# Kernel optimization log

Hardware: AMD Instinct MI355X
Metric: run time of the kernel (lower is better)

## Reference

```python
import jax, jax.numpy as jnp
import numpy as np

N, Lq, Lk = 4, 4096, 4096
H, P = 16, 128
D = H * P  # 2048


def setup_inputs() -> dict:
    key = jax.random.key(0)
    ks = jax.random.split(key, 7)
    s = 1.0 / np.sqrt(D).astype(np.float32)
    query = jax.random.normal(ks[0], (N, Lq, D), jnp.float32)
    key_t = jax.random.normal(ks[1], (N, Lk, D), jnp.float32)
    Wq = jax.random.normal(ks[2], (D, D), jnp.float32) * s
    Wk = jax.random.normal(ks[3], (D, D), jnp.float32) * s
    Wv = jax.random.normal(ks[4], (D, D), jnp.float32) * s
    query_padding_mask = jax.random.uniform(ks[5], (N, Lq)) < 0.1
    key_padding_mask = jax.random.uniform(ks[6], (N, Lk)) < 0.1
    return {"query": query, "key": key_t, "Wq": Wq, "Wk": Wk, "Wv": Wv,
            "query_padding_mask": query_padding_mask,
            "key_padding_mask": key_padding_mask}


def reference(query, key, Wq, Wk, Wv, query_padding_mask, key_padding_mask):
    n, lq, _ = query.shape
    lk = key.shape[1]
    # torch.nn.Linear(bias=False): y = x @ W^T; split into heads -> (N,H,L,P)
    q = (query @ Wq.T).reshape(n, lq, H, P).transpose(0, 2, 1, 3)
    k = (key @ Wk.T).reshape(n, lk, H, P).transpose(0, 2, 1, 3)
    v = (key @ Wv.T).reshape(n, lk, H, P).transpose(0, 2, 1, 3)
    # _log_exp_kernel(x) = log(1 + exp(x)) = softplus
    pq = jax.nn.softplus(q)
    pk = jax.nn.softplus(k)
    # zero out padded keys so they contribute nothing to numerator/denominator
    pk = jnp.where(key_padding_mask[:, None, :, None], 0.0, pk)
    # linear attention: O(L*d^2) instead of O(L^2*d)
    kv = jnp.einsum("nhkd,nhke->nhde", pk, v)          # (N,H,P,P)
    num = jnp.einsum("nhqd,nhde->nhqe", pq, kv)        # (N,H,Lq,P)
    den = jnp.einsum("nhqd,nhd->nhq", pq, pk.sum(axis=2))[..., None]
    att = num / den
    out = att.transpose(0, 2, 1, 3).reshape(n, lq, H * P)
    # zero out padded query positions
    out = jnp.where(query_padding_mask[..., None], 0.0, out)
    return out
```

## Files before the change

kernel.cpp:

```cpp
#include <hip/hip_runtime.h>
#include <stdint.h>

typedef __attribute__((ext_vector_type(8))) short    bh8;
typedef __attribute__((ext_vector_type(4))) float    fx4;
typedef __attribute__((ext_vector_type(4))) float    f4v;
typedef unsigned short u16;
typedef __attribute__((ext_vector_type(4))) unsigned short u16x4;

#define DEV static __device__ __forceinline__

DEV u16 f2bf(float f) {
  unsigned u = __float_as_uint(f);
  u += 0x7FFFu + ((u >> 16) & 1u);
  return (u16)(u >> 16);
}
DEV float bf2f(u16 s) { return __uint_as_float(((unsigned)s) << 16); }
DEV float softplus_f(float x) { return fmaxf(x, 0.f) + log1pf(expf(-fabsf(x))); }

DEV void gload_lds16(const u16* g, u16* l) {
  __builtin_amdgcn_global_load_lds(
      (const __attribute__((address_space(1))) unsigned int*)g,
      (__attribute__((address_space(3))) unsigned int*)l, 16, 0, 0);
}
DEV void stage2(const u16* s, u16* d) {
  gload_lds16(s, d);
  gload_lds16(s + 131072, d + 4096);
}

__global__ __launch_bounds__(256) void k_cvt(const float* __restrict__ in,
                                             u16* __restrict__ out, int n4) {
  int i = blockIdx.x * 256 + threadIdx.x;
  int stride = gridDim.x * 256;
  for (; i < n4; i += stride) {
    f4v v = ((const f4v*)in)[i];
    u16x4 o;
    o.x = f2bf(v.x); o.y = f2bf(v.y); o.z = f2bf(v.z); o.w = f2bf(v.w);
    ((u16x4*)out)[i] = o;
  }
}


#define MM(a, b, c) __builtin_amdgcn_mfma_f32_16x16x32_bf16(a, b, c, 0, 0, 0)
#define LD(BASE, RR, KS) \
  (*(const bh8*)&lsg[(BASE) + (RR) * 64 + ((((KS) * 32) + ko8) ^ swz)])

#define DECLQ(Q)                                                          \
  fx4 acc##Q##00 = {}, acc##Q##01 = {}, acc##Q##10 = {}, acc##Q##11 = {}, \
      acc##Q##20 = {}, acc##Q##21 = {}, acc##Q##30 = {}, acc##Q##31 = {}

#define WN
#define WV6 asm volatile("s_waitcnt vmcnt(6)");
#define WV4 asm volatile("s_waitcnt vmcnt(4)");

#define LDA4(AB, KS)                                                     \
  a_0##KS = LD(AB, arow0,      KS); a_1##KS = LD(AB, arow0 + 16, KS);    \
  a_2##KS = LD(AB, arow0 + 32, KS); a_3##KS = LD(AB, arow0 + 48, KS);

#define LDB2(BN, BB, KS)                                                 \
  b##BN##_0##KS = LD(BB, brow0,      KS);                                \
  b##BN##_1##KS = LD(BB, brow0 + 16, KS);

#define MFMA8(Q, BN, KS)                                                 \
  acc##Q##00 = MM(a_0##KS, b##BN##_0##KS, acc##Q##00);                   \
  acc##Q##01 = MM(a_0##KS, b##BN##_1##KS, acc##Q##01);                   \
  acc##Q##10 = MM(a_1##KS, b##BN##_0##KS, acc##Q##10);                   \
  acc##Q##11 = MM(a_1##KS, b##BN##_1##KS, acc##Q##11);                   \
  acc##Q##20 = MM(a_2##KS, b##BN##_0##KS, acc##Q##20);                   \
  acc##Q##21 = MM(a_2##KS, b##BN##_1##KS, acc##Q##21);                   \
  acc##Q##30 = MM(a_3##KS, b##BN##_0##KS, acc##Q##30);                   \
  acc##Q##31 = MM(a_3##KS, b##BN##_1##KS, acc##Q##31);

#define PH(MFMAS, WAITS, ...) {                 \
  __VA_ARGS__                                   \
  __builtin_amdgcn_s_barrier();                 \
  __builtin_amdgcn_s_setprio(1);                \
  MFMAS                                         \
  __builtin_amdgcn_s_setprio(0);                \
  WAITS                                         \
  __builtin_amdgcn_s_barrier();                 \
}

#define STE(AC, EL, JOFF) {                                                   \
  float v = AC.EL;                                                            \
  if (EPI >= 1) v = softplus_f(v);                                            \
  if (EPI == 2) { if (mask[gi0 + JOFF]) v = 0.f; }                            \
  C[(size_t)(gi0 + JOFF) * 2048 + gj] = f2bf(v);                              \
}
#define ST1(AC, QR, QC, MI, NI) {                                             \
  int gi0 = bm0 + (QR) * 128 + wr * 64 + (MI) * 16 + (lane >> 4) * 4;         \
  int gj  = bn0 + (QC) * 128 + wc * 32 + (NI) * 16 + l15;                     \
  STE(AC, x, 0) STE(AC, y, 1) STE(AC, z, 2) STE(AC, w, 3)                     \
}
#define EPIQ(Q, QR, QC)                                                       \
  ST1(acc##Q##00, QR, QC, 0, 0) ST1(acc##Q##01, QR, QC, 0, 1)                 \
  ST1(acc##Q##10, QR, QC, 1, 0) ST1(acc##Q##11, QR, QC, 1, 1)                 \
  ST1(acc##Q##20, QR, QC, 2, 0) ST1(acc##Q##21, QR, QC, 2, 1)                 \
  ST1(acc##Q##30, QR, QC, 3, 0) ST1(acc##Q##31, QR, QC, 3, 1)

template <int EPI>
__global__ __launch_bounds__(512, 2) void k_gemm256(
    const u16* __restrict__ A, const u16* __restrict__ B, u16* __restrict__ C,
    const int* __restrict__ mask) {
  extern __shared__ u16 lsg[];
  int tid = threadIdx.x, lane = tid & 63, wid = tid >> 6;
  int xcd = blockIdx.x & 7, i = blockIdx.x >> 3;
  int bm0 = (xcd * 8 + (i & 7)) << 8;
  int bn0 = (i >> 3) << 8;
  int wr = wid >> 2, wc = wid & 3;
  int l15 = lane & 15, ko8 = (lane >> 4) * 8;
  int swz = (l15 & 7) << 3;
  int arow0 = wr * 64 + l15, brow0 = wc * 32 + l15;
  int lr = lane >> 3, cg = (lane & 7) ^ lr;
  const u16* srcA = A + (size_t)(bm0 + wid * 8 + lr) * 2048 + cg * 8;
  const u16* srcB = B + (size_t)(bn0 + wid * 8 + lr) * 2048 + cg * 8;
  u16* lsu = lsg + wid * 512;

  DECLQ(0); DECLQ(1); DECLQ(2); DECLQ(3);
  bh8 a_00 = {}, a_01 = {}, a_10 = {}, a_11 = {},
      a_20 = {}, a_21 = {}, a_30 = {}, a_31 = {};
  bh8 b0_00 = {}, b0_01 = {}, b0_10 = {}, b0_11 = {};
  bh8 b1_00 = {}, b1_01 = {}, b1_10 = {}, b1_11 = {};

  stage2(srcA, lsu + 0);
  stage2(srcB, lsu + 16384);
  stage2(srcB + 262144, lsu + 24576);
  stage2(srcA + 262144, lsu + 8192);
  stage2(srcA + 64, lsu + 32768);
  stage2(srcB + 64, lsu + 49152);
  stage2(srcB + 262144 + 64, lsu + 57344);
  asm volatile("s_waitcnt vmcnt(8)");
  __builtin_amdgcn_s_barrier();
  LDA4(0, 0) LDB2(0, 16384, 0) LDB2(1, 24576, 0)

  for (int it = 0; it < 16; it++) {
    int t1 = 2 * it + 1;
    int t2 = (2 * it + 2) & 31;
    int t3 = (2 * it + 3) & 31;
    PH(MFMA8(0, 0, 0) MFMA8(1, 1, 0), WV6,
       LDA4(0, 1) LDB2(0, 16384, 1) LDB2(1, 24576, 1))
    PH(MFMA8(0, 0, 1) MFMA8(1, 1, 1), WN,
       LDA4(8192, 0) stage2(srcA + 262144 + t1 * 64, lsu + 40960);)
    PH(MFMA8(2, 0, 0) MFMA8(3, 1, 0), WV4,
       LDA4(8192, 1) stage2(srcA + t2 * 64, lsu + 0);)
    PH(MFMA8(2, 0, 1) MFMA8(3, 1, 1), WN,
       LDA4(32768, 0) LDB2(0, 49152, 0) LDB2(1, 57344, 0)
       stage2(srcB + t2 * 64, lsu + 16384);)
    PH(MFMA8(0, 0, 0) MFMA8(1, 1, 0), WV6,
       LDA4(32768, 1) LDB2(0, 49152, 1) LDB2(1, 57344, 1)
       stage2(srcB + 262144 + t2 * 64, lsu + 24576);)
    PH(MFMA8(0, 0, 1) MFMA8(1, 1, 1), WN,
       LDA4(40960, 0) stage2(srcA + 262144 + t2 * 64, lsu + 8192);)
    PH(MFMA8(2, 0, 0) MFMA8(3, 1, 0), WV6,
       LDA4(40960, 1) stage2(srcA + t3 * 64, lsu + 32768);
       stage2(srcB + t3 * 64, lsu + 49152);)
    PH(MFMA8(2, 0, 1) MFMA8(3, 1, 1), WN,
       LDA4(0, 0) LDB2(0, 16384, 0) LDB2(1, 24576, 0)
       stage2(srcB + 262144 + t3 * 64, lsu + 57344);)
  }

  EPIQ(0, 0, 0)
  EPIQ(1, 0, 1)
  EPIQ(2, 1, 0)
  EPIQ(3, 1, 1)
}

__global__ __launch_bounds__(256, 2) void k_kv2(const u16* __restrict__ pk,
                                                const u16* __restrict__ v,
                                                float* __restrict__ part,
                                                float* __restrict__ spart) {
  int nh = blockIdx.x >> 3, slab = blockIdx.x & 7;
  int n = nh >> 4, h = nh & 15;
  __shared__ u16 lsA[128 * 32];
  __shared__ u16 lsB[128 * 32];
  __shared__ float redS[32][128];
  int tid = threadIdx.x, lane = tid & 63, wid = tid >> 6;
  int wr = wid >> 1, wc = wid & 1;
  int kk = tid >> 3;
  int dg = (tid & 7) * 16;
  size_t rowbase = ((size_t)(n * 4096 + slab * 512) + kk) * 2048 + h * 128 + dg;
  int r = lane & 15, ko = (lane >> 4) * 8;
  fx4 acc[4][4] = {};
  float sA[16];
#pragma unroll
  for (int i = 0; i < 16; i++) sA[i] = 0.f;
  for (int k0 = 0; k0 < 512; k0 += 32) {
    __syncthreads();
    bh8 a0 = *(const bh8*)(pk + rowbase + (size_t)k0 * 2048);
    bh8 a1 = *(const bh8*)(pk + rowbase + (size_t)k0 * 2048 + 8);
    bh8 b0 = *(const bh8*)(v + rowbase + (size_t)k0 * 2048);
    bh8 b1 = *(const bh8*)(v + rowbase + (size_t)k0 * 2048 + 8);
#pragma unroll
    for (int i = 0; i < 8; i++) {
      sA[i] += bf2f((u16)a0[i]);
      sA[8 + i] += bf2f((u16)a1[i]);
    }
#pragma unroll
    for (int i = 0; i < 8; i++) {
      lsA[(dg + i) * 32 + kk] = (u16)a0[i];
      lsA[(dg + 8 + i) * 32 + kk] = (u16)a1[i];
      lsB[(dg + i) * 32 + kk] = (u16)b0[i];
      lsB[(dg + 8 + i) * 32 + kk] = (u16)b1[i];
    }
    __syncthreads();
    bh8 af[4], bfr[4];
#pragma unroll
    for (int mi = 0; mi < 4; mi++)
      af[mi] = *(const bh8*)&lsA[(wr * 64 + mi * 16 + r) * 32 + ko];
#pragma unroll
    for (int ni = 0; ni < 4; ni++)
      bfr[ni] = *(const bh8*)&lsB[(wc * 64 + ni * 16 + r) * 32 + ko];
#pragma unroll
    for (int mi = 0; mi < 4; mi++)
#pragma unroll
      for (int ni = 0; ni < 4; ni++)
        acc[mi][ni] = __builtin_amdgcn_mfma_f32_16x16x32_bf16(af[mi], bfr[ni],
                                                              acc[mi][ni], 0, 0, 0);
  }
#pragma unroll
  for (int mi = 0; mi < 4; mi++)
#pragma unroll
    for (int ni = 0; ni < 4; ni++)
#pragma unroll
      for (int j = 0; j < 4; j++) {
        int d = wr * 64 + mi * 16 + (lane >> 4) * 4 + j;
        int e = wc * 64 + ni * 16 + (lane & 15);
        part[(size_t)blockIdx.x * 16384 + e * 128 + d] = acc[mi][ni][j];
      }
#pragma unroll
  for (int i = 0; i < 16; i++) redS[kk][dg + i] = sA[i];
  __syncthreads();
  if (tid < 128) {
    float s = 0.f;
#pragma unroll
    for (int p = 0; p < 32; p++) s += redS[p][tid];
    spart[blockIdx.x * 128 + tid] = s;
  }
}

__global__ __launch_bounds__(256) void k_red(const float* __restrict__ part,
                                             const float* __restrict__ spart,
                                             u16* __restrict__ kvT,
                                             float* __restrict__ sb) {
  int nh = blockIdx.x, tid = threadIdx.x;
  for (int i = tid; i < 16384; i += 256) {
    float s = 0.f;
#pragma unroll
    for (int sl = 0; sl < 8; sl++) s += part[(size_t)(nh * 8 + sl) * 16384 + i];
    kvT[(size_t)nh * 16384 + i] = f2bf(s);
  }
  if (tid < 128) {
    float s = 0.f;
#pragma unroll
    for (int sl = 0; sl < 8; sl++) s += spart[(nh * 8 + sl) * 128 + tid];
    sb[nh * 128 + tid] = s;
  }
}

__global__ __launch_bounds__(256, 2) void k_att(
    const u16* __restrict__ pq, const u16* __restrict__ kvT,
    const float* __restrict__ s, const int* __restrict__ qmask,
    float* __restrict__ out) {
  int b = blockIdx.x;
  int lt = b & 31, h = (b >> 5) & 15, nb = b >> 9;
  int l0 = lt * 128;
  __shared__ u16 lsQ[128 * 128];
  __shared__ u16 lsKV[128 * 128];
  __shared__ float lsS[128];
  __shared__ float lsDen[128];
  int tid = threadIdx.x, lane = tid & 63, wid = tid >> 6;

  int row = tid >> 1, part = tid & 1;
  const u16* gq = pq + ((size_t)(nb * 4096 + l0 + row)) * 2048 + h * 128 + part * 64;
  const u16* gk = kvT + ((size_t)(nb * 16 + h) * 128 + row) * 128 + part * 64;
  int sw = (row & 7) << 3;
#pragma unroll
  for (int j = 0; j < 8; j++) {
    bh8 vq = *(const bh8*)(gq + j * 8);
    bh8 vk = *(const bh8*)(gk + j * 8);
    int ci = (part * 64 + j * 8) ^ sw;
    *(bh8*)&lsQ[row * 128 + ci] = vq;
    *(bh8*)&lsKV[row * 128 + ci] = vk;
  }
  if (tid < 128) lsS[tid] = s[(nb * 16 + h) * 128 + tid];
  __syncthreads();

  if (tid < 128) {
    int rr = tid, swr = (rr & 7) << 3;
    float dsum = 0.f;
    for (int dd = 0; dd < 128; dd++) {
      int d = (dd + rr) & 127;
      dsum += bf2f(lsQ[rr * 128 + (d ^ swr)]) * lsS[d];
    }
    lsDen[rr] = dsum;
  }
  __syncthreads();

  int wr = wid >> 1, wc = wid & 1;
  int r = lane & 15, ko = (lane >> 4) * 8;
  fx4 acc[4][4] = {};
#pragma unroll
  for (int ks = 0; ks < 4; ks++) {
    bh8 af[4], bfr[4];
#pragma unroll
    for (int mi = 0; mi < 4; mi++) {
      int rw = wr * 64 + mi * 16 + r;
      af[mi] = *(const bh8*)&lsQ[rw * 128 + ((ks * 32 + ko) ^ ((rw & 7) << 3))];
    }
#pragma unroll
    for (int ni = 0; ni < 4; ni++) {
      int rw = wc * 64 + ni * 16 + r;
      bfr[ni] = *(const bh8*)&lsKV[rw * 128 + ((ks * 32 + ko) ^ ((rw & 7) << 3))];
    }
#pragma unroll
    for (int mi = 0; mi < 4; mi++)
#pragma unroll
      for (int ni = 0; ni < 4; ni++)
        acc[mi][ni] = __builtin_amdgcn_mfma_f32_16x16x32_bf16(af[mi], bfr[ni],
                                                              acc[mi][ni], 0, 0, 0);
  }
#pragma unroll
  for (int mi = 0; mi < 4; mi++)
#pragma unroll
    for (int ni = 0; ni < 4; ni++)
#pragma unroll
      for (int j = 0; j < 4; j++) {
        int li = wr * 64 + mi * 16 + (lane >> 4) * 4 + j;
        int e = wc * 64 + ni * 16 + (lane & 15);
        int l = l0 + li;
        float v = qmask[nb * 4096 + l] ? 0.f : acc[mi][ni][j] / lsDen[li];
        out[((size_t)(nb * 4096 + l)) * 2048 + h * 128 + e] = v;
      }
}

extern "C" void kernel_launch(void* const* d_in, const int* in_sizes, int n_in,
                              void* d_out, int out_size, void* d_ws, size_t ws_size,
                              hipStream_t stream) {
  const float* query = (const float*)d_in[0];
  const float* key   = (const float*)d_in[1];
  const float* Wq    = (const float*)d_in[2];
  const float* Wk    = (const float*)d_in[3];
  const float* Wv    = (const float*)d_in[4];
  const int* qmask   = (const int*)d_in[5];
  const int* kmask   = (const int*)d_in[6];
  float* out = (float*)d_out;
  char* ws = (char*)d_ws;

  u16* qb   = (u16*)(ws + 0);
  u16* kb   = (u16*)(ws + 67108864ull);
  u16* Wqb  = (u16*)(ws + 134217728ull);
  u16* Wkb  = (u16*)(ws + 142606336ull);
  u16* Wvb  = (u16*)(ws + 150994944ull);
  u16* pq   = (u16*)(ws + 159383552ull);
  u16* kvT  = (u16*)(ws + 226492416ull);
  float* sb = (float*)(ws + 228589568ull);
  float* kvpart = (float*)(ws + 0);
  float* spart  = (float*)(ws + 33554432ull);
  u16* pk = (u16*)d_out;
  u16* vb = (u16*)d_out + 33554432ull;

  k_cvt<<<2048, 256, 0, stream>>>(query, qb, 33554432 / 4);
  k_cvt<<<2048, 256, 0, stream>>>(key, kb, 33554432 / 4);
  k_cvt<<<512, 256, 0, stream>>>(Wq, Wqb, 4194304 / 4);
  k_cvt<<<512, 256, 0, stream>>>(Wk, Wkb, 4194304 / 4);
  k_cvt<<<512, 256, 0, stream>>>(Wv, Wvb, 4194304 / 4);

  k_gemm256<1><<<512, 512, 131072, stream>>>(qb, Wqb, pq, nullptr);
  k_gemm256<2><<<512, 512, 131072, stream>>>(kb, Wkb, pk, kmask);
  k_gemm256<0><<<512, 512, 131072, stream>>>(kb, Wvb, vb, nullptr);

  k_kv2<<<512, 256, 0, stream>>>(pk, vb, kvpart, spart);
  k_red<<<64, 256, 0, stream>>>(kvpart, spart, kvT, sb);
  k_att<<<2048, 256, 0, stream>>>(pq, kvT, sb, qmask, out);
}
```

Measured before the change: 741.5 us.

## Restructure GEMM main loop into four larger phases with coarser prefetch

Reorganizes the 256x256 bf16 GEMM pipeline from eight half-k phases into four phases. Each phase loads both k-slices of fragments from LDS and then issues 32 MFMAs. The global-to-LDS staging is regrouped per half-tile, and the prologue now waits for all loads to finish instead of prefetching the next tile. This halves the barrier count per iteration and lengthens the MFMA runs. In exchange, more fragment registers are live at once, the wait-count accounting is new, and LDS-read latency is less hidden behind MFMAs.

```diff
diff --git a/kernel.cpp b/kernel.cpp
--- a/kernel.cpp
+++ b/kernel.cpp
@@ -48,9 +48,14 @@
   fx4 acc##Q##00 = {}, acc##Q##01 = {}, acc##Q##10 = {}, acc##Q##11 = {}, \
       acc##Q##20 = {}, acc##Q##21 = {}, acc##Q##30 = {}, acc##Q##31 = {}
 
-#define WN
+#define DECLFRAGS                                                         \
+  bh8 a_00 = {}, a_01 = {}, a_10 = {}, a_11 = {},                         \
+      a_20 = {}, a_21 = {}, a_30 = {}, a_31 = {};                         \
+  bh8 b0_00 = {}, b0_01 = {}, b0_10 = {}, b0_11 = {};                     \
+  bh8 b1_00 = {}, b1_01 = {}, b1_10 = {}, b1_11 = {};
+
 #define WV6 asm volatile("s_waitcnt vmcnt(6)");
-#define WV4 asm volatile("s_waitcnt vmcnt(4)");
+#define WV2 asm volatile("s_waitcnt vmcnt(2)");
 
 #define LDA4(AB, KS)                                                     \
   a_0##KS = LD(AB, arow0,      KS); a_1##KS = LD(AB, arow0 + 16, KS);    \
@@ -70,13 +75,13 @@
   acc##Q##30 = MM(a_3##KS, b##BN##_0##KS, acc##Q##30);                   \
   acc##Q##31 = MM(a_3##KS, b##BN##_1##KS, acc##Q##31);
 
-#define PH(MFMAS, WAITS, ...) {                 \
+#define PH4(MFMAS, WAIT, ...) {                 \
   __VA_ARGS__                                   \
   __builtin_amdgcn_s_barrier();                 \
   __builtin_amdgcn_s_setprio(1);                \
   MFMAS                                         \
   __builtin_amdgcn_s_setprio(0);                \
-  WAITS                                         \
+  WAIT                                          \
   __builtin_amdgcn_s_barrier();                 \
 }
 
@@ -116,46 +121,36 @@
   u16* lsu = lsg + wid * 512;
 
   DECLQ(0); DECLQ(1); DECLQ(2); DECLQ(3);
-  bh8 a_00 = {}, a_01 = {}, a_10 = {}, a_11 = {},
-      a_20 = {}, a_21 = {}, a_30 = {}, a_31 = {};
-  bh8 b0_00 = {}, b0_01 = {}, b0_10 = {}, b0_11 = {};
-  bh8 b1_00 = {}, b1_01 = {}, b1_10 = {}, b1_11 = {};
+  DECLFRAGS
 
   stage2(srcA, lsu + 0);
   stage2(srcB, lsu + 16384);
   stage2(srcB + 262144, lsu + 24576);
   stage2(srcA + 262144, lsu + 8192);
-  stage2(srcA + 64, lsu + 32768);
-  stage2(srcB + 64, lsu + 49152);
-  stage2(srcB + 262144 + 64, lsu + 57344);
-  asm volatile("s_waitcnt vmcnt(8)");
+  asm volatile("s_waitcnt vmcnt(0)");
   __builtin_amdgcn_s_barrier();
-  LDA4(0, 0) LDB2(0, 16384, 0) LDB2(1, 24576, 0)
 
   for (int it = 0; it < 16; it++) {
-    int t1 = 2 * it + 1;
-    int t2 = (2 * it + 2) & 31;
-    int t3 = (2 * it + 3) & 31;
-    PH(MFMA8(0, 0, 0) MFMA8(1, 1, 0), WV6,
-       LDA4(0, 1) LDB2(0, 16384, 1) LDB2(1, 24576, 1))
-    PH(MFMA8(0, 0, 1) MFMA8(1, 1, 1), WN,
-       LDA4(8192, 0) stage2(srcA + 262144 + t1 * 64, lsu + 40960);)
-    PH(MFMA8(2, 0, 0) MFMA8(3, 1, 0), WV4,
-       LDA4(8192, 1) stage2(srcA + t2 * 64, lsu + 0);)
-    PH(MFMA8(2, 0, 1) MFMA8(3, 1, 1), WN,
-       LDA4(32768, 0) LDB2(0, 49152, 0) LDB2(1, 57344, 0)
-       stage2(srcB + t2 * 64, lsu + 16384);)
-    PH(MFMA8(0, 0, 0) MFMA8(1, 1, 0), WV6,
-       LDA4(32768, 1) LDB2(0, 49152, 1) LDB2(1, 57344, 1)
-       stage2(srcB + 262144 + t2 * 64, lsu + 24576);)
-    PH(MFMA8(0, 0, 1) MFMA8(1, 1, 1), WN,
-       LDA4(40960, 0) stage2(srcA + 262144 + t2 * 64, lsu + 8192);)
-    PH(MFMA8(2, 0, 0) MFMA8(3, 1, 0), WV6,
-       LDA4(40960, 1) stage2(srcA + t3 * 64, lsu + 32768);
-       stage2(srcB + t3 * 64, lsu + 49152);)
-    PH(MFMA8(2, 0, 1) MFMA8(3, 1, 1), WN,
-       LDA4(0, 0) LDB2(0, 16384, 0) LDB2(1, 24576, 0)
-       stage2(srcB + 262144 + t3 * 64, lsu + 57344);)
+    int tO = 2 * it + 1;
+    int tE = (2 * it + 2) & 31;
+    PH4(MFMA8(0, 0, 0) MFMA8(1, 1, 0) MFMA8(0, 0, 1) MFMA8(1, 1, 1), WV6,
+        LDA4(0, 0) LDB2(0, 16384, 0) LDB2(1, 24576, 0)
+        LDA4(0, 1) LDB2(0, 16384, 1) LDB2(1, 24576, 1)
+        stage2(srcA + tO * 64, lsu + 32768);
+        stage2(srcB + tO * 64, lsu + 49152);
+        stage2(srcB + 262144 + tO * 64, lsu + 57344);)
+    PH4(MFMA8(2, 0, 0) MFMA8(3, 1, 0) MFMA8(2, 0, 1) MFMA8(3, 1, 1), WV2,
+        LDA4(8192, 0) LDA4(8192, 1)
+        stage2(srcA + 262144 + tO * 64, lsu + 40960);)
+    PH4(MFMA8(0, 0, 0) MFMA8(1, 1, 0) MFMA8(0, 0, 1) MFMA8(1, 1, 1), WV6,
+        LDA4(32768, 0) LDB2(0, 49152, 0) LDB2(1, 57344, 0)
+        LDA4(32768, 1) LDB2(0, 49152, 1) LDB2(1, 57344, 1)
+        stage2(srcA + tE * 64, lsu + 0);
+        stage2(srcB + tE * 64, lsu + 16384);
+        stage2(srcB + 262144 + tE * 64, lsu + 24576);)
+    PH4(MFMA8(2, 0, 0) MFMA8(3, 1, 0) MFMA8(2, 0, 1) MFMA8(3, 1, 1), WV2,
+        LDA4(40960, 0) LDA4(40960, 1)
+        stage2(srcA + 262144 + tE * 64, lsu + 8192);)
   }
 
   EPIQ(0, 0, 0)
```

Result: no change. 743.7 us (+0.3%).
